# Kernel tuning notes

Hardware: AMD Instinct MI355X
Metric: run time of the kernel (lower is better)

## Reference

```python
import jax, jax.numpy as jnp
import numpy as np

N = 100000      # nodes
E = 1600000     # edges (avg degree 16)
D_IN = 128
D_OUT = 64
N_SCALES = 3
DEPTH = 10
TELEPORTS = np.array([0.1, 0.2, 0.3], dtype=np.float32)


def setup_inputs() -> dict:
    key = jax.random.key(0)
    ks = jax.random.split(key, 9)
    data = jax.random.normal(ks[0], (N, D_IN), dtype=jnp.float32)
    src = jax.random.randint(ks[1], (E,), 0, N, dtype=jnp.int32)
    tgt = jax.random.randint(ks[2], (E,), 0, N, dtype=jnp.int32)
    s = 1.0 / np.sqrt(D_IN)
    Ws = jax.random.uniform(ks[3], (N_SCALES, D_IN, D_OUT), jnp.float32, -s, s)
    bs = jax.random.uniform(ks[4], (N_SCALES, D_OUT), jnp.float32, -s, s)
    W_src = jax.random.uniform(ks[5], (D_IN, D_OUT), jnp.float32, -s, s)
    b_src = jax.random.uniform(ks[6], (D_OUT,), jnp.float32, -s, s)
    so = 1.0 / np.sqrt(D_OUT)
    W_tgt = jax.random.uniform(ks[7], (D_OUT, D_OUT), jnp.float32, -so, so)
    b_tgt = jax.random.uniform(ks[8], (D_OUT,), jnp.float32, -so, so)
    return {"data": data, "src": src, "tgt": tgt, "Ws": Ws, "bs": bs,
            "W_src": W_src, "b_src": b_src, "W_tgt": W_tgt, "b_tgt": b_tgt}


def reference(data, src, tgt, Ws, bs, W_src, b_src, W_tgt, b_tgt):
    # per-target-node degree (indices.unique counts repeated per edge)
    deg = jax.ops.segment_sum(jnp.ones((E,), jnp.float32), tgt, num_segments=N)
    deg_inv = 1.0 / jnp.maximum(deg, 1.0)           # [N]
    edge_w = deg_inv[tgt][:, None]                  # [E,1] normalized factor

    def laplacian(x):                               # x: [N, D_OUT]
        diff = (x[tgt] - x[src]) * edge_w           # (own - source_message)/deg
        return jax.ops.segment_sum(diff, tgt, num_segments=N)

    lap3 = jax.vmap(laplacian)                      # over scale dim

    t = jnp.asarray(TELEPORTS)[:, None, None]       # [S,1,1]
    emb = jnp.einsum('nd,sdo->sno', data, Ws) + bs[:, None, :]   # [S,N,O]
    out = emb
    for _ in range(DEPTH):
        out = (1.0 - t) * lap3(out) + t * emb
    scales = jax.nn.relu(out)                       # [S,N,O]

    s_att = data @ W_src + b_src                    # [N,O]
    t_att = jnp.einsum('sno,op->snp', scales, W_tgt) + b_tgt     # [S,N,O]
    logits = jnp.einsum('snp,np->sn', t_att, s_att)              # [S,N]
    att = jax.nn.softmax(logits, axis=0)            # softmax over scales
    return jnp.einsum('sn,sno->no', att, scales)    # [N,O]
```

## Files before the change

### kernel.cpp

```cpp
#include <hip/hip_runtime.h>
#include <hip/hip_bf16.h>

#define NN   100000
#define EE   1600000
#define CAP  48
#define NT   6250
#define NPB  192
#define NB   521

typedef __attribute__((ext_vector_type(8))) short bf16x8;
typedef __attribute__((ext_vector_type(4))) float f32x4;

__device__ inline short f2b_rne(float f) {
  union { float f; unsigned u; } x; x.f = f;
  unsigned r = x.u + 0x7fffu + ((x.u >> 16) & 1u);
  return (short)(r >> 16);
}
__device__ inline unsigned pack_rne(float lo, float hi) {
  unsigned ul = __float_as_uint(lo); ul += 0x7fffu + ((ul >> 16) & 1u);
  unsigned uh = __float_as_uint(hi); uh += 0x7fffu + ((uh >> 16) & 1u);
  return __builtin_amdgcn_perm(uh, ul, 0x07060302u);
}
__device__ inline float lo2f(unsigned u) { return __uint_as_float(u << 16); }
__device__ inline float hi2f(unsigned u) { return __uint_as_float(u & 0xffff0000u); }
__device__ inline float b2f(unsigned short u) { return __uint_as_float((unsigned)u << 16); }

__global__ __launch_bounds__(256) void k_fillA(const int* __restrict__ tgt,
                                               int* __restrict__ ghist) {
  __shared__ int h[NB];
  for (int i = threadIdx.x; i < NB; i += 256) h[i] = 0;
  __syncthreads();
  int e = blockIdx.x * 4096 + threadIdx.x;
#pragma unroll
  for (int k = 0; k < 16; ++k, e += 256)
    if (e < EE) atomicAdd(&h[tgt[e] / NPB], 1);
  __syncthreads();
  for (int i = threadIdx.x; i < NB; i += 256)
    if (h[i]) atomicAdd(&ghist[i], h[i]);
}

__global__ __launch_bounds__(256) void k_scan(const int* __restrict__ ghist,
                                              int* __restrict__ base,
                                              int* __restrict__ tail) {
  __shared__ int v[1024];
  const int tid = threadIdx.x;
  for (int i = tid; i < 1024; i += 256) v[i] = (i < NB) ? ghist[i] : 0;
  __syncthreads();
  for (int off = 1; off < 1024; off <<= 1) {
    int tmp[4];
#pragma unroll
    for (int j = 0; j < 4; ++j) {
      int i = tid + j * 256;
      tmp[j] = (i >= off) ? v[i - off] : 0;
    }
    __syncthreads();
#pragma unroll
    for (int j = 0; j < 4; ++j) v[tid + j * 256] += tmp[j];
    __syncthreads();
  }
  for (int i = tid; i <= NB; i += 256) {
    int bb = (i == 0) ? 0 : v[i - 1];
    base[i] = bb;
    if (i < NB) tail[i] = bb;
  }
}

__global__ __launch_bounds__(256) void k_fillB(const int* __restrict__ tgt,
                                               const int* __restrict__ src,
                                               int* tail, uint2* __restrict__ part) {
  __shared__ int hist[NB], cur[NB], basel[NB];
  const int tid = threadIdx.x;
  for (int i = tid; i < NB; i += 256) { hist[i] = 0; cur[i] = 0; }
  __syncthreads();
  const int e0 = blockIdx.x * 4096 + tid;
  int tv[16], sv[16];
#pragma unroll
  for (int k = 0; k < 16; ++k) {
    int e = e0 + k * 256;
    tv[k] = -1;
    if (e < EE) {
      tv[k] = tgt[e]; sv[k] = src[e];
      atomicAdd(&hist[tv[k] / NPB], 1);
    }
  }
  __syncthreads();
  for (int b = tid; b < NB; b += 256)
    if (hist[b]) basel[b] = atomicAdd(&tail[b], hist[b]);
  __syncthreads();
#pragma unroll
  for (int k = 0; k < 16; ++k) {
    if (tv[k] >= 0) {
      int b = tv[k] / NPB;
      int r = atomicAdd(&cur[b], 1);
      part[basel[b] + r] = make_uint2((unsigned)sv[k], (unsigned)tv[k]);
    }
  }
}

__global__ __launch_bounds__(256) void k_fillC(const int* __restrict__ base,
                                               const uint2* __restrict__ part,
                                               int* __restrict__ cnt,
                                               int* __restrict__ col) {
  __shared__ int ccnt[NPB];
  __shared__ int ccol[NPB * CAP];
  const int b = blockIdx.x, tid = threadIdx.x;
  for (int i = tid; i < NPB; i += 256) ccnt[i] = 0;
  __syncthreads();
  const int lo = base[b], hi = base[b + 1];
  for (int i = lo + tid; i < hi; i += 256) {
    uint2 e = part[i];
    int nl = (int)e.y - b * NPB;
    int p = atomicAdd(&ccnt[nl], 1);
    if (p < CAP) ccol[nl * CAP + p] = (int)e.x;
  }
  __syncthreads();
  const int n0 = b * NPB;
  for (int i = tid; i < NPB; i += 256)
    if (n0 + i < NN) cnt[n0 + i] = ccnt[i];
  for (int i = tid; i < NPB * CAP; i += 256) {
    int n = n0 + i / CAP;
    if (n < NN) col[(size_t)n0 * CAP + i] = ccol[i];
  }
}

__global__ void k_cast(const float* __restrict__ data, unsigned* __restrict__ y0) {
  int i = blockIdx.x * 256 + threadIdx.x;
  const float2 v = ((const float2*)data)[i];
  y0[i] = pack_rne(v.x, v.y);
}

__global__ __launch_bounds__(256) void k_weff(
    const float* __restrict__ Wsrc, const float* __restrict__ bsrc,
    const float* __restrict__ Wtgt, float* __restrict__ Weff,
    float* __restrict__ beff) {
  const int i = blockIdx.x * 256 + threadIdx.x;
  if (i < 8192) {
    const int d = i >> 6, o = i & 63;
    float s = 0.f;
#pragma unroll
    for (int p = 0; p < 64; ++p) s = fmaf(Wsrc[d * 64 + p], Wtgt[o * 64 + p], s);
    Weff[i] = s;
  } else if (i < 8256) {
    const int o = i - 8192;
    float s = 0.f;
#pragma unroll
    for (int p = 0; p < 64; ++p) s = fmaf(bsrc[p], Wtgt[o * 64 + p], s);
    beff[o] = s;
  }
}

template <int MODE>
__global__ __launch_bounds__(256) void k_prop(
    const int* __restrict__ cnt, const int* __restrict__ col,
    const unsigned* __restrict__ xin, unsigned* xout,
    const unsigned* s0p, const unsigned* s1p,
    unsigned* __restrict__ z0, unsigned* __restrict__ z1,
    unsigned* __restrict__ z2,
    float4 g0, float4 g1, float4 g2) {
  const int wv = threadIdx.x >> 6, lane = threadIdx.x & 63;
  const int n = blockIdx.x * 4 + wv;
  if (n >= NN) return;
  const size_t p = (size_t)n * 64 + lane;
  const int d = cnt[n];
  const int dm = (d < CAP) ? d : CAP;
  int idx = (lane < dm) ? col[n * CAP + lane] : 0;
  const unsigned own = xin[p];
  unsigned S0 = 0, S1 = 0, U0 = 0, U1 = 0, U2 = 0;
  if (MODE == 1 || MODE == 2 || MODE == 3) S0 = s0p[p];
  if (MODE == 1 || MODE == 2) S1 = s1p[p];
  if (MODE == 2 || MODE == 3) { U0 = z0[p]; U1 = z1[p]; U2 = z2[p]; }

  float s0 = 0.f, s1 = 0.f;
  int i = 0;
  for (; i + 8 <= dm; i += 8) {
    int j0 = __builtin_amdgcn_readlane(idx, i);
    int j1 = __builtin_amdgcn_readlane(idx, i + 1);
    int j2 = __builtin_amdgcn_readlane(idx, i + 2);
    int j3 = __builtin_amdgcn_readlane(idx, i + 3);
    int j4 = __builtin_amdgcn_readlane(idx, i + 4);
    int j5 = __builtin_amdgcn_readlane(idx, i + 5);
    int j6 = __builtin_amdgcn_readlane(idx, i + 6);
    int j7 = __builtin_amdgcn_readlane(idx, i + 7);
    unsigned a0 = xin[(size_t)j0 * 64 + lane];
    unsigned a1 = xin[(size_t)j1 * 64 + lane];
    unsigned a2 = xin[(size_t)j2 * 64 + lane];
    unsigned a3 = xin[(size_t)j3 * 64 + lane];
    unsigned a4 = xin[(size_t)j4 * 64 + lane];
    unsigned a5 = xin[(size_t)j5 * 64 + lane];
    unsigned a6 = xin[(size_t)j6 * 64 + lane];
    unsigned a7 = xin[(size_t)j7 * 64 + lane];
    s0 += ((lo2f(a0) + lo2f(a1)) + (lo2f(a2) + lo2f(a3))) +
          ((lo2f(a4) + lo2f(a5)) + (lo2f(a6) + lo2f(a7)));
    s1 += ((hi2f(a0) + hi2f(a1)) + (hi2f(a2) + hi2f(a3))) +
          ((hi2f(a4) + hi2f(a5)) + (hi2f(a6) + hi2f(a7)));
  }
  for (; i + 2 <= dm; i += 2) {
    int j0 = __builtin_amdgcn_readlane(idx, i);
    int j1 = __builtin_amdgcn_readlane(idx, i + 1);
    unsigned a0 = xin[(size_t)j0 * 64 + lane];
    unsigned a1 = xin[(size_t)j1 * 64 + lane];
    s0 += lo2f(a0) + lo2f(a1);
    s1 += hi2f(a0) + hi2f(a1);
  }
  if (i < dm) {
    int j0 = __builtin_amdgcn_readlane(idx, i);
    unsigned a0 = xin[(size_t)j0 * 64 + lane];
    s0 += lo2f(a0); s1 += hi2f(a0);
  }
  const float gate = (d > 0) ? 1.f : 0.f;
  const float inv  = (d > 0) ? 1.f / (float)d : 0.f;
  const float o0 = lo2f(own), o1 = hi2f(own);
  const float l0 = gate * (o0 - inv * s0);
  const float l1 = gate * (o1 - inv * s1);
  if (MODE != 3) xout[p] = pack_rne(l0, l1);
  if (MODE == 1 || MODE == 2) {
    const float a0 = lo2f(S0), a1 = hi2f(S0), b0 = lo2f(S1), b1 = hi2f(S1);
    float t0lo = g0.x * a0 + g0.y * b0 + g0.z * o0 + g0.w * l0;
    float t0hi = g0.x * a1 + g0.y * b1 + g0.z * o1 + g0.w * l1;
    float t1lo = g1.x * a0 + g1.y * b0 + g1.z * o0 + g1.w * l0;
    float t1hi = g1.x * a1 + g1.y * b1 + g1.z * o1 + g1.w * l1;
    float t2lo = g2.x * a0 + g2.y * b0 + g2.z * o0 + g2.w * l0;
    float t2hi = g2.x * a1 + g2.y * b1 + g2.z * o1 + g2.w * l1;
    if (MODE == 2) {
      t0lo += lo2f(U0); t0hi += hi2f(U0);
      t1lo += lo2f(U1); t1hi += hi2f(U1);
      t2lo += lo2f(U2); t2hi += hi2f(U2);
    }
    z0[p] = pack_rne(t0lo, t0hi);
    z1[p] = pack_rne(t1lo, t1hi);
    z2[p] = pack_rne(t2lo, t2hi);
  } else if (MODE == 3) {
    const float a0 = lo2f(S0), a1 = hi2f(S0);
    z0[p] = pack_rne(lo2f(U0) + g0.x * a0 + g0.z * o0 + g0.w * l0,
                     hi2f(U0) + g0.x * a1 + g0.z * o1 + g0.w * l1);
    z1[p] = pack_rne(lo2f(U1) + g1.x * a0 + g1.z * o0 + g1.w * l0,
                     hi2f(U1) + g1.x * a1 + g1.z * o1 + g1.w * l1);
    z2[p] = pack_rne(lo2f(U2) + g2.x * a0 + g2.z * o0 + g2.w * l0,
                     hi2f(U2) + g2.x * a1 + g2.z * o1 + g2.w * l1);
  }
}

__global__ __launch_bounds__(256) void k_gemm2(
    const unsigned* __restrict__ z0, const unsigned* __restrict__ z1,
    const unsigned* __restrict__ z2, const unsigned* __restrict__ y0,
    const float* __restrict__ Ws, const float* __restrict__ bs,
    const float* __restrict__ Weff, const float* __restrict__ beff,
    __hip_bfloat16* __restrict__ scales, unsigned short* __restrict__ m) {
  const int lane = threadIdx.x & 63;
  const int wv   = threadIdx.x >> 6;
  const int n16  = lane & 15;
  const int q    = lane >> 4;
  const unsigned* Ab = (wv == 0) ? z0 : (wv == 1) ? z1 : (wv == 2) ? z2 : y0;
  const float tw = 0.1f * (float)(wv + 1);

  bf16x8 Bf[4][4];
  float  bias[4];
#pragma unroll
  for (int ct = 0; ct < 4; ++ct) {
    const int c = ct * 16 + n16;
    const float* bp = (wv < 3) ? (Ws + (size_t)wv * 8192 + c) : (Weff + c);
    bias[ct] = (wv < 3) ? tw * bs[wv * 64 + c] : beff[c];
#pragma unroll
    for (int s = 0; s < 4; ++s) {
      const int k0 = s * 32 + q * 8;
      union { short h[8]; bf16x8 v; } u;
#pragma unroll
      for (int j = 0; j < 8; ++j) u.h[j] = f2b_rne(bp[(size_t)(k0 + j) * 64]);
      Bf[ct][s] = u.v;
    }
  }

  for (int t = blockIdx.x; t < NT; t += gridDim.x) {
    const int row = t * 16 + n16;
    const uint4* ap = (const uint4*)(Ab + (size_t)row * 64);
    f32x4 acc[4];
#pragma unroll
    for (int ct = 0; ct < 4; ++ct)
      acc[ct] = (f32x4){bias[ct], bias[ct], bias[ct], bias[ct]};
#pragma unroll
    for (int s = 0; s < 4; ++s) {
      union { uint4 u; bf16x8 v; } af;
      af.u = ap[s * 4 + q];
#pragma unroll
      for (int ct = 0; ct < 4; ++ct)
        acc[ct] = __builtin_amdgcn_mfma_f32_16x16x32_bf16(af.v, Bf[ct][s], acc[ct], 0, 0, 0);
    }
    if (wv < 3) {
#pragma unroll
      for (int ct = 0; ct < 4; ++ct) {
        const int c = wv * 64 + ct * 16 + n16;
#pragma unroll
        for (int i = 0; i < 4; ++i) {
          const int r = t * 16 + q * 4 + i;
          scales[(size_t)r * 192 + c] = __float2bfloat16(acc[ct][i]);
        }
      }
    } else {
#pragma unroll
      for (int ct = 0; ct < 4; ++ct) {
        const int c = ct * 16 + n16;
#pragma unroll
        for (int i = 0; i < 4; ++i) {
          const int r = t * 16 + q * 4 + i;
          m[(size_t)r * 64 + c] = (unsigned short)f2b_rne(acc[ct][i]);
        }
      }
    }
  }
}

__global__ __launch_bounds__(256) void k_att2(
    const unsigned short* __restrict__ scales,
    const unsigned short* __restrict__ m, float* __restrict__ io) {
  const int wv = threadIdx.x >> 6, lane = threadIdx.x & 63;
  for (int n = blockIdx.x * 4 + wv; n < NN; n += gridDim.x * 4) {
    const unsigned short* sr = scales + (size_t)n * 192;
    float v0 = fmaxf(b2f(sr[lane]), 0.f);
    float v1 = fmaxf(b2f(sr[64 + lane]), 0.f);
    float v2 = fmaxf(b2f(sr[128 + lane]), 0.f);
    float mm = b2f(m[(size_t)n * 64 + lane]);
    float l0 = v0 * mm, l1 = v1 * mm, l2 = v2 * mm;
#pragma unroll
    for (int off = 32; off; off >>= 1) {
      l0 += __shfl_xor(l0, off);
      l1 += __shfl_xor(l1, off);
      l2 += __shfl_xor(l2, off);
    }
    float mx = fmaxf(l0, fmaxf(l1, l2));
    float x0 = __expf(l0 - mx), x1 = __expf(l1 - mx), x2 = __expf(l2 - mx);
    float invs = 1.f / (x0 + x1 + x2);
    io[(size_t)n * 64 + lane] = (x0 * v0 + x1 * v1 + x2 * v2) * invs;
  }
}

extern "C" void kernel_launch(void* const* d_in, const int* in_sizes, int n_in,
                              void* d_out, int out_size, void* d_ws, size_t ws_size,
                              hipStream_t stream) {
  (void)in_sizes; (void)n_in; (void)out_size; (void)ws_size;
  const float* data = (const float*)d_in[0];
  const int*   srcp = (const int*)d_in[1];
  const int*   tgtp = (const int*)d_in[2];
  const float* Ws   = (const float*)d_in[3];
  const float* bs   = (const float*)d_in[4];
  const float* Wsrc = (const float*)d_in[5];
  const float* bsrc = (const float*)d_in[6];
  const float* Wtgt = (const float*)d_in[7];
  float* out = (float*)d_out;

  char* ws = (char*)d_ws;
  auto al = [](size_t x) { return (x + 255) & ~(size_t)255; };
  size_t off = 0;
  auto take = [&](size_t bytes) { size_t o = off; off += al(bytes); return o; };
  int*      cnt   = (int*)(ws + take((size_t)NN * 4));
  int*      col   = (int*)(ws + take((size_t)NN * CAP * 4));
  int*      ghist = (int*)(ws + take((size_t)NB * 4));
  int*      base  = (int*)(ws + take((size_t)(NB + 1) * 4));
  int*      tail  = (int*)(ws + take((size_t)NB * 4));
  float*    Weff  = (float*)(ws + take((size_t)8192 * 4));
  float*    beff  = (float*)(ws + take((size_t)64 * 4));
  uint2*    part  = (uint2*)(ws + take((size_t)EE * 8));
  const size_t szY = (size_t)NN * 64 * 4;
  unsigned* Y0 = (unsigned*)(ws + take(szY));
  unsigned* R1 = (unsigned*)(ws + take(szY));
  unsigned* R2 = (unsigned*)(ws + take(szY));
  unsigned* R3 = (unsigned*)(ws + take(szY));
  unsigned* z0 = (unsigned*)(ws + take(szY));
  unsigned* z1 = (unsigned*)(ws + take(szY));
  unsigned* z2 = (unsigned*)(ws + take(szY));
  __hip_bfloat16* scales = (__hip_bfloat16*)R2;
  unsigned short* mbuf   = (unsigned short*)R1;

  float c[3][11];
  for (int s = 0; s < 3; ++s) {
    float t = 0.1f * (float)(s + 1), pw = 1.f;
    for (int j = 0; j < 10; ++j) { c[s][j] = t * pw; pw *= (1.f - t); }
    c[s][10] = pw;
  }
  float4 A3[3], A7[3], A10[3];
  for (int s = 0; s < 3; ++s) {
    A3[s]  = make_float4(c[s][0], c[s][1], c[s][2], c[s][3]);
    A7[s]  = make_float4(c[s][4], c[s][5], c[s][6], c[s][7]);
    A10[s] = make_float4(c[s][8], 0.f,     c[s][9], c[s][10]);
  }
  const float4 Zf = make_float4(0.f, 0.f, 0.f, 0.f);

  const int EB = (EE + 4095) / 4096;
  hipMemsetAsync(ghist, 0, NB * 4, stream);
  k_fillA<<<EB, 256, 0, stream>>>(tgtp, ghist);
  k_scan<<<1, 256, 0, stream>>>(ghist, base, tail);
  k_fillB<<<EB, 256, 0, stream>>>(tgtp, srcp, tail, part);
  k_fillC<<<NB, 256, 0, stream>>>(base, part, cnt, col);
  k_cast<<<NN * 64 / 256, 256, 0, stream>>>(data, Y0);
  k_weff<<<33, 256, 0, stream>>>(Wsrc, bsrc, Wtgt, Weff, beff);

  const int PG = (NN + 3) / 4;
  k_prop<0><<<PG, 256, 0, stream>>>(cnt, col, Y0, R1, nullptr, nullptr,
      nullptr, nullptr, nullptr, Zf, Zf, Zf);
  k_prop<0><<<PG, 256, 0, stream>>>(cnt, col, R1, R2, nullptr, nullptr,
      nullptr, nullptr, nullptr, Zf, Zf, Zf);
  k_prop<1><<<PG, 256, 0, stream>>>(cnt, col, R2, R3, Y0, R1,
      z0, z1, z2, A3[0], A3[1], A3[2]);
  k_prop<0><<<PG, 256, 0, stream>>>(cnt, col, R3, R1, nullptr, nullptr,
      nullptr, nullptr, nullptr, Zf, Zf, Zf);
  k_prop<0><<<PG, 256, 0, stream>>>(cnt, col, R1, R2, nullptr, nullptr,
      nullptr, nullptr, nullptr, Zf, Zf, Zf);
  k_prop<0><<<PG, 256, 0, stream>>>(cnt, col, R2, R3, nullptr, nullptr,
      nullptr, nullptr, nullptr, Zf, Zf, Zf);
  k_prop<2><<<PG, 256, 0, stream>>>(cnt, col, R3, R1, R1, R2,
      z0, z1, z2, A7[0], A7[1], A7[2]);
  k_prop<0><<<PG, 256, 0, stream>>>(cnt, col, R1, R2, nullptr, nullptr,
      nullptr, nullptr, nullptr, Zf, Zf, Zf);
  k_prop<0><<<PG, 256, 0, stream>>>(cnt, col, R2, R3, nullptr, nullptr,
      nullptr, nullptr, nullptr, Zf, Zf, Zf);
  k_prop<3><<<PG, 256, 0, stream>>>(cnt, col, R3, nullptr, R2, nullptr,
      z0, z1, z2, A10[0], A10[1], A10[2]);

  k_gemm2<<<512, 256, 0, stream>>>(z0, z1, z2, Y0, Ws, bs, Weff, beff,
                                   scales, mbuf);
  k_att2<<<6250, 256, 0, stream>>>((const unsigned short*)scales, mbuf, out);
}
```

Before: 879.1 us.

## Chunk feature layout into 8 column slabs for cache-friendly propagation gathers

Stores the 128-wide bf16 feature rows as 8 separate column chunks of 16 features (32 bytes per node per chunk). Propagation blocks now handle one chunk for 32 nodes, with 8 lanes per node, and loop over neighbors with per-lane index loads and masked accumulation. The aim is to shrink each chunk's gather working set so it fits in L2/MALL and raises hit rates. In exchange, every gather is now a 32-byte segment instead of a full 256-byte row, neighbor indices are re-read 8 times, and warps run divergent loops over varying degrees; the cast and GEMM kernels are updated to read the new layout.

```diff
diff --git a/kernel.cpp b/kernel.cpp
--- a/kernel.cpp
+++ b/kernel.cpp
@@ -7,6 +7,7 @@
 #define NT   6250
 #define NPB  192
 #define NB   521
+#define NGB  3125
 
 typedef __attribute__((ext_vector_type(8))) short bf16x8;
 typedef __attribute__((ext_vector_type(4))) float f32x4;
@@ -124,9 +125,12 @@
 }
 
 __global__ void k_cast(const float* __restrict__ data, unsigned* __restrict__ y0) {
-  int i = blockIdx.x * 256 + threadIdx.x;
-  const float2 v = ((const float2*)data)[i];
-  y0[i] = pack_rne(v.x, v.y);
+  int o = blockIdx.x * 256 + threadIdx.x;
+  int f = o & 7;
+  int n = (o >> 3) % NN;
+  int c = o / (NN * 8);
+  const float2 v = *(const float2*)(data + (size_t)n * 128 + c * 16 + f * 2);
+  y0[o] = pack_rne(v.x, v.y);
 }
 
 __global__ __launch_bounds__(256) void k_weff(
@@ -157,61 +161,41 @@
     unsigned* __restrict__ z0, unsigned* __restrict__ z1,
     unsigned* __restrict__ z2,
     float4 g0, float4 g1, float4 g2) {
+  const int c  = blockIdx.x / NGB;
+  const int g  = blockIdx.x % NGB;
   const int wv = threadIdx.x >> 6, lane = threadIdx.x & 63;
-  const int n = blockIdx.x * 4 + wv;
-  if (n >= NN) return;
-  const size_t p = (size_t)n * 64 + lane;
-  const int d = cnt[n];
+  const int e  = lane >> 3, f = lane & 7;
+  const int n  = g * 32 + wv * 8 + e;
+  const size_t cb = (size_t)c * (NN * 8);
+  const size_t p  = cb + (size_t)n * 8 + f;
+  const int d  = cnt[n];
   const int dm = (d < CAP) ? d : CAP;
-  int idx = (lane < dm) ? col[n * CAP + lane] : 0;
   const unsigned own = xin[p];
   unsigned S0 = 0, S1 = 0, U0 = 0, U1 = 0, U2 = 0;
   if (MODE == 1 || MODE == 2 || MODE == 3) S0 = s0p[p];
   if (MODE == 1 || MODE == 2) S1 = s1p[p];
   if (MODE == 2 || MODE == 3) { U0 = z0[p]; U1 = z1[p]; U2 = z2[p]; }
 
-  float s0 = 0.f, s1 = 0.f;
-  int i = 0;
-  for (; i + 8 <= dm; i += 8) {
-    int j0 = __builtin_amdgcn_readlane(idx, i);
-    int j1 = __builtin_amdgcn_readlane(idx, i + 1);
-    int j2 = __builtin_amdgcn_readlane(idx, i + 2);
-    int j3 = __builtin_amdgcn_readlane(idx, i + 3);
-    int j4 = __builtin_amdgcn_readlane(idx, i + 4);
-    int j5 = __builtin_amdgcn_readlane(idx, i + 5);
-    int j6 = __builtin_amdgcn_readlane(idx, i + 6);
-    int j7 = __builtin_amdgcn_readlane(idx, i + 7);
-    unsigned a0 = xin[(size_t)j0 * 64 + lane];
-    unsigned a1 = xin[(size_t)j1 * 64 + lane];
-    unsigned a2 = xin[(size_t)j2 * 64 + lane];
-    unsigned a3 = xin[(size_t)j3 * 64 + lane];
-    unsigned a4 = xin[(size_t)j4 * 64 + lane];
-    unsigned a5 = xin[(size_t)j5 * 64 + lane];
-    unsigned a6 = xin[(size_t)j6 * 64 + lane];
-    unsigned a7 = xin[(size_t)j7 * 64 + lane];
-    s0 += ((lo2f(a0) + lo2f(a1)) + (lo2f(a2) + lo2f(a3))) +
-          ((lo2f(a4) + lo2f(a5)) + (lo2f(a6) + lo2f(a7)));
-    s1 += ((hi2f(a0) + hi2f(a1)) + (hi2f(a2) + hi2f(a3))) +
-          ((hi2f(a4) + hi2f(a5)) + (hi2f(a6) + hi2f(a7)));
-  }
-  for (; i + 2 <= dm; i += 2) {
-    int j0 = __builtin_amdgcn_readlane(idx, i);
-    int j1 = __builtin_amdgcn_readlane(idx, i + 1);
-    unsigned a0 = xin[(size_t)j0 * 64 + lane];
-    unsigned a1 = xin[(size_t)j1 * 64 + lane];
-    s0 += lo2f(a0) + lo2f(a1);
-    s1 += hi2f(a0) + hi2f(a1);
-  }
-  if (i < dm) {
-    int j0 = __builtin_amdgcn_readlane(idx, i);
-    unsigned a0 = xin[(size_t)j0 * 64 + lane];
-    s0 += lo2f(a0); s1 += hi2f(a0);
+  const int* cl = col + (size_t)n * CAP;
+  float slo = 0.f, shi = 0.f;
+  for (int i = 0; i < CAP; i += 4) {
+    if (__ballot(i < dm) == 0ull) break;
+#pragma unroll
+    for (int k = 0; k < 4; ++k) {
+      const int ii = i + k;
+      const bool act = ii < dm;
+      const int j = act ? cl[ii] : n;
+      const unsigned a = xin[cb + (size_t)j * 8 + f];
+      const float m = act ? 1.f : 0.f;
+      slo = fmaf(m, lo2f(a), slo);
+      shi = fmaf(m, hi2f(a), shi);
+    }
   }
   const float gate = (d > 0) ? 1.f : 0.f;
   const float inv  = (d > 0) ? 1.f / (float)d : 0.f;
   const float o0 = lo2f(own), o1 = hi2f(own);
-  const float l0 = gate * (o0 - inv * s0);
-  const float l1 = gate * (o1 - inv * s1);
+  const float l0 = gate * (o0 - inv * slo);
+  const float l1 = gate * (o1 - inv * shi);
   if (MODE != 3) xout[p] = pack_rne(l0, l1);
   if (MODE == 1 || MODE == 2) {
     const float a0 = lo2f(S0), a1 = hi2f(S0), b0 = lo2f(S1), b1 = hi2f(S1);
@@ -272,15 +256,16 @@
 
   for (int t = blockIdx.x; t < NT; t += gridDim.x) {
     const int row = t * 16 + n16;
-    const uint4* ap = (const uint4*)(Ab + (size_t)row * 64);
     f32x4 acc[4];
 #pragma unroll
     for (int ct = 0; ct < 4; ++ct)
       acc[ct] = (f32x4){bias[ct], bias[ct], bias[ct], bias[ct]};
 #pragma unroll
     for (int s = 0; s < 4; ++s) {
+      const int dw = s * 16 + q * 4;
+      const int cc = dw >> 3, ff = dw & 7;
       union { uint4 u; bf16x8 v; } af;
-      af.u = ap[s * 4 + q];
+      af.u = *(const uint4*)(Ab + (size_t)cc * (NN * 8) + (size_t)row * 8 + ff);
 #pragma unroll
       for (int ct = 0; ct < 4; ++ct)
         acc[ct] = __builtin_amdgcn_mfma_f32_16x16x32_bf16(af.v, Bf[ct][s], acc[ct], 0, 0, 0);
@@ -393,7 +378,7 @@
   k_cast<<<NN * 64 / 256, 256, 0, stream>>>(data, Y0);
   k_weff<<<33, 256, 0, stream>>>(Wsrc, bsrc, Wtgt, Weff, beff);
 
-  const int PG = (NN + 3) / 4;
+  const int PG = 8 * NGB;
   k_prop<0><<<PG, 256, 0, stream>>>(cnt, col, Y0, R1, nullptr, nullptr,
       nullptr, nullptr, nullptr, Zf, Zf, Zf);
   k_prop<0><<<PG, 256, 0, stream>>>(cnt, col, R1, R2, nullptr, nullptr,
```

After: 1.799 ms. 105% more time.
